# Optimization experiments

Measured on AMD Instinct MI355X. Metric: run time of the kernel, lower is better.

## Reference

```python
import jax, jax.numpy as jnp
import numpy as np

B, S, HID = 2, 4096, 2048
NH, NKV, HD = 16, 4, 128  # num_heads, num_kv_heads, head_dim
GROUPS = NH // NKV
ROPE_THETA = 10000.0


def _rope_cos_sin(position_ids):
    # position_ids: [B, S] int
    inv_freq = 1.0 / (ROPE_THETA ** (jnp.arange(0, HD, 2, dtype=jnp.float32) / HD))  # [HD/2]
    freqs = position_ids.astype(jnp.float32)[..., None] * inv_freq  # [B, S, HD/2]
    emb = jnp.concatenate([freqs, freqs], axis=-1)  # [B, S, HD]
    return jnp.cos(emb), jnp.sin(emb)


def _rotate_half(x):
    x1, x2 = jnp.split(x, 2, axis=-1)
    return jnp.concatenate([-x2, x1], axis=-1)


def _apply_rope(q, k, cos, sin):
    # q: [B, NH, S, HD], k: [B, NKV, S, HD]; cos/sin: [B, S, HD]
    cos = cos[:, None, :, :]
    sin = sin[:, None, :, :]
    q = q * cos + _rotate_half(q) * sin
    k = k * cos + _rotate_half(k) * sin
    return q, k


def kappa(x):
    return jax.nn.elu(x) + 1.0


def setup_inputs() -> dict:
    key = jax.random.key(0)
    ks = jax.random.split(key, 8)
    sc = 0.02
    hidden_states = jax.random.normal(ks[0], (B, S, HID), dtype=jnp.float32)
    position_ids = jnp.broadcast_to(jnp.arange(S, dtype=jnp.int64)[None, :], (B, S))
    Wq = jax.random.normal(ks[1], (HID, NH * HD), dtype=jnp.float32) * sc
    Wk = jax.random.normal(ks[2], (HID, NKV * HD), dtype=jnp.float32) * sc
    Wv = jax.random.normal(ks[3], (HID, NKV * HD), dtype=jnp.float32) * sc
    Wo = jax.random.normal(ks[4], (HID, HID), dtype=jnp.float32) * sc
    Wphi = jax.random.normal(ks[5], (HID, HID), dtype=jnp.float32) * sc
    bphi = jax.random.normal(ks[6], (HID,), dtype=jnp.float32) * sc
    return {"hidden_states": hidden_states, "position_ids": position_ids,
            "Wq": Wq, "Wk": Wk, "Wv": Wv, "Wo": Wo, "Wphi": Wphi, "bphi": bphi}


def reference(hidden_states, position_ids, Wq, Wk, Wv, Wo, Wphi, bphi):
    b, s, _ = hidden_states.shape
    # projections -> [B, heads, S, HD]
    q = (hidden_states @ Wq).reshape(b, s, NH, HD).transpose(0, 2, 1, 3)
    k = (hidden_states @ Wk).reshape(b, s, NKV, HD).transpose(0, 2, 1, 3)
    v = (hidden_states @ Wv).reshape(b, s, NKV, HD).transpose(0, 2, 1, 3)
    cos, sin = _rope_cos_sin(position_ids)
    q, k = _apply_rope(q, k, cos, sin)
    # GQA expand kv heads
    k = jnp.repeat(k, GROUPS, axis=1)  # [B, NH, S, HD]
    v = jnp.repeat(v, GROUPS, axis=1)
    Qk = kappa(q)
    Kk = kappa(k)
    Qg = Qk.mean(axis=2)  # [B, NH, HD]
    logits = jnp.einsum('bnd,bnsd->bns', Qg, Kk)
    alpha = jax.nn.softmax(logits, axis=-1) * float(s)  # [B, NH, S]
    outer_sum = jnp.einsum('bns,bnsd,bnsf->bndf', alpha, Kk, v)  # [B, NH, HD, HD]
    X_phi = (hidden_states @ Wphi + bphi).reshape(b, s, NH, HD).transpose(0, 2, 1, 3)
    result_attn = jnp.einsum('bnsd,bndf->bnsf', Qk, outer_sum)
    context = (X_phi * result_attn).transpose(0, 2, 1, 3).reshape(b, s, HID)
    return context @ Wo
```

## Files before the change

kernel.cpp:

```cpp
#include <hip/hip_runtime.h>
#include <hip/hip_bf16.h>
#include <math.h>

#define B_    2
#define S_    4096
#define HID_  2048
#define NH_   16
#define NKV_  4
#define HD_   128
#define GROUPS_ (NH_/NKV_)
#define ROPE_THETA_ 10000.0f
#define OSPLIT 8
#define QCH   32

typedef __attribute__((ext_vector_type(8))) short short8;
typedef __attribute__((ext_vector_type(4))) float f32x4;

__device__ inline unsigned short f2bf(float f) {
    __hip_bfloat16 h = __float2bfloat16(f);
    return *(unsigned short*)&h;
}

__device__ inline float bf2f(short u) {
    union { unsigned int i; float f; } v;
    v.i = ((unsigned int)(unsigned short)u) << 16;
    return v.f;
}

__device__ inline void gload16(const void* g, void* l) {
    __builtin_amdgcn_global_load_lds((const __attribute__((address_space(1))) void*)g,
                                     (__attribute__((address_space(3))) void*)l, 16, 0, 0);
}

#define BARM() asm volatile("s_barrier" ::: "memory")

__global__ void rope_table_kernel(float* __restrict__ cosT, float* __restrict__ sinT) {
    int s = blockIdx.x;
    int i = threadIdx.x;
    float expo = -2.0f * (float)i / (float)HD_;
    float invf = powf(ROPE_THETA_, expo);
    float f = (float)s * invf;
    cosT[s * 64 + i] = cosf(f);
    sinT[s * 64 + i] = sinf(f);
}

__global__ void cast_bf16_kernel(const float* __restrict__ in,
                                 __hip_bfloat16* __restrict__ out, int n8) {
    int i = blockIdx.x * 256 + threadIdx.x;
    if (i >= n8) return;
    const float4 v0 = *reinterpret_cast<const float4*>(&in[i * 8]);
    const float4 v1 = *reinterpret_cast<const float4*>(&in[i * 8 + 4]);
    union { short8 v; unsigned short u[8]; } o;
    o.u[0] = f2bf(v0.x); o.u[1] = f2bf(v0.y); o.u[2] = f2bf(v0.z); o.u[3] = f2bf(v0.w);
    o.u[4] = f2bf(v1.x); o.u[5] = f2bf(v1.y); o.u[6] = f2bf(v1.z); o.u[7] = f2bf(v1.w);
    *reinterpret_cast<short8*>(&out[i * 8]) = o.v;
}

__global__ __launch_bounds__(256) void transpose_cast_all_kernel(
        const float* __restrict__ Wq, const float* __restrict__ Wphi,
        const float* __restrict__ Wk, const float* __restrict__ Wv,
        const float* __restrict__ Wo, __hip_bfloat16* __restrict__ dstBase) {
    __shared__ float T[64][65];
    int id = blockIdx.x;
    const float* W; int N; size_t dof;
    if (id < 1024)      { W = Wq;   N = 2048; dof = 0; }
    else if (id < 2048) { W = Wphi; N = 2048; dof = (size_t)2048 * HID_;        id -= 1024; }
    else if (id < 2304) { W = Wk;   N = 512;  dof = (size_t)4096 * HID_;        id -= 2048; }
    else if (id < 2560) { W = Wv;   N = 512;  dof = (size_t)(4096 + 512) * HID_; id -= 2304; }
    else                { W = Wo;   N = 2048; dof = (size_t)5120 * HID_;        id -= 2560; }
    __hip_bfloat16* Wt = dstBase + dof;
    int nb = N >> 6;
    int n0 = (id % nb) * 64, k0 = (id / nb) * 64;
    int tid = threadIdx.x;
    int r = tid >> 4, c4 = (tid & 15) * 4;
#pragma unroll
    for (int p = 0; p < 4; ++p) {
        float4 v = *reinterpret_cast<const float4*>(&W[(size_t)(k0 + r + p * 16) * N + n0 + c4]);
        T[r + p * 16][c4 + 0] = v.x;
        T[r + p * 16][c4 + 1] = v.y;
        T[r + p * 16][c4 + 2] = v.z;
        T[r + p * 16][c4 + 3] = v.w;
    }
    __syncthreads();
#pragma unroll
    for (int p = 0; p < 4; ++p) {
        int n = r + p * 16;
        short4 o;
        o.x = (short)f2bf(T[c4 + 0][n]);
        o.y = (short)f2bf(T[c4 + 1][n]);
        o.z = (short)f2bf(T[c4 + 2][n]);
        o.w = (short)f2bf(T[c4 + 3][n]);
        *reinterpret_cast<short4*>(&Wt[(size_t)(n0 + n) * HID_ + k0 + c4]) = o;
    }
}

__device__ __forceinline__ void stage_region128(const __hip_bfloat16* __restrict__ src,
        int ldK, int row0, int kbase, __hip_bfloat16* dst, int tid) {
#pragma unroll
    for (int g = 0; g < 2; ++g) {
        int P = g * 256 + tid;
        int row = P >> 2, cp = P & 3;
        int cl = cp ^ ((row >> 1) & 3);
        gload16(src + (size_t)(row0 + row) * ldK + kbase + cl * 8, dst + P * 8);
    }
}

#define BM 128
#define BN 128
#define T128EL 8192
__global__ __launch_bounds__(256) void gemm_mfma_kernel(
        const __hip_bfloat16* __restrict__ A, const __hip_bfloat16* __restrict__ Bt,
        __hip_bfloat16* __restrict__ Cb, int M, int N, int K) {
    __shared__ __hip_bfloat16 lds[4 * T128EL];
    int tid  = threadIdx.x;
    int wid  = tid >> 6, lane = tid & 63;
    int wr   = wid >> 1, wc = wid & 1;
    int lr = lane & 15, lc = lane >> 4;
    int c16 = lc ^ ((lr >> 1) & 3);
    int bm = blockIdx.y * BM, bn = blockIdx.x * BN;

    f32x4 acc[4][4];
#pragma unroll
    for (int m = 0; m < 4; ++m)
#pragma unroll
        for (int n = 0; n < 4; ++n)
#pragma unroll
            for (int i = 0; i < 4; ++i) acc[m][n][i] = 0.0f;

    const int NKT = K >> 5;

    stage_region128(A,  K, bm, 0,  lds,                 tid);
    stage_region128(Bt, K, bn, 0,  lds + 4096,          tid);
    stage_region128(A,  K, bm, 32, lds + T128EL,        tid);
    stage_region128(Bt, K, bn, 32, lds + T128EL + 4096, tid);
    asm volatile("s_waitcnt vmcnt(4)" ::: "memory");
    BARM();

    for (int kt = 0; kt < NKT; ++kt) {
        __hip_bfloat16* buf = lds + (size_t)(kt & 3) * T128EL;
        __hip_bfloat16* stg = lds + (size_t)((kt + 2) & 3) * T128EL;
        const bool pf = (kt + 2 < NKT);
        if (pf) {
            stage_region128(A,  K, bm, (kt + 2) << 5, stg,        tid);
            stage_region128(Bt, K, bn, (kt + 2) << 5, stg + 4096, tid);
        }
        short8 af[4], bf[4];
#pragma unroll
        for (int m = 0; m < 4; ++m)
            af[m] = *reinterpret_cast<const short8*>(
                &buf[(size_t)(wr * 64 + m * 16 + lr) * 32 + c16 * 8]);
#pragma unroll
        for (int n = 0; n < 4; ++n)
            bf[n] = *reinterpret_cast<const short8*>(
                &buf[4096 + (size_t)(wc * 64 + n * 16 + lr) * 32 + c16 * 8]);
        __builtin_amdgcn_s_setprio(1);
#pragma unroll
        for (int m = 0; m < 4; ++m)
#pragma unroll
            for (int n = 0; n < 4; ++n)
                acc[m][n] = __builtin_amdgcn_mfma_f32_16x16x32_bf16(
                    af[m], bf[n], acc[m][n], 0, 0, 0);
        __builtin_amdgcn_s_setprio(0);
        if (pf) { asm volatile("s_waitcnt vmcnt(4)" ::: "memory"); }
        else    { asm volatile("s_waitcnt vmcnt(0)" ::: "memory"); }
        BARM();
    }

    int lq = lane >> 4;
#pragma unroll
    for (int m = 0; m < 4; ++m) {
#pragma unroll
        for (int n = 0; n < 4; ++n) {
            int row = bm + wr * 64 + m * 16 + lq * 4;
            int col = bn + wc * 64 + n * 16 + lr;
#pragma unroll
            for (int r = 0; r < 4; ++r)
                Cb[(size_t)(row + r) * N + col] = __float2bfloat16(acc[m][n][r]);
        }
    }
}

#define HBUF 32768

__device__ __forceinline__ void stageA64(const __hip_bfloat16* __restrict__ A,
        int ldK, int bm, int k0, __hip_bfloat16* dst, int g, int tid) {
    int P = g * 512 + tid;
    int row = P >> 3, sp = P & 7;
    gload16(A + (size_t)(bm + row) * ldK + k0 + ((sp ^ (row & 7)) << 3),
            dst + (size_t)P * 8);
}
__device__ __forceinline__ void stageB64(const __hip_bfloat16* __restrict__ Bt,
        int ldK, int bn, int k0, __hip_bfloat16* dst, int g, int tid) {
    int P = g * 512 + tid;
    int row = P >> 3, sp = P & 7;
    gload16(Bt + (size_t)(bn + row) * ldK + k0 + ((sp ^ (row & 7)) << 3),
            dst + 16384 + (size_t)P * 8);
}

__device__ __forceinline__ short8 ldsA64(const __hip_bfloat16* buf, int row, int slot_log) {
    int sp = slot_log ^ (row & 7);
    return *reinterpret_cast<const short8*>(&buf[(size_t)row * 64 + sp * 8]);
}
__device__ __forceinline__ short8 ldsB64(const __hip_bfloat16* buf, int row, int slot_log) {
    int sp = slot_log ^ (row & 7);
    return *reinterpret_cast<const short8*>(&buf[16384 + (size_t)row * 64 + sp * 8]);
}

__global__ __launch_bounds__(512, 2) void gemm_mfma256_kernel(
        const __hip_bfloat16* __restrict__ A, const __hip_bfloat16* __restrict__ Bt,
        float* __restrict__ C, __hip_bfloat16* __restrict__ CbQ,
        __hip_bfloat16* __restrict__ CbP, const float* __restrict__ bias,
        int M, int N, int K) {
    __shared__ __hip_bfloat16 lds[2 * HBUF];
    int tid = threadIdx.x, lane = tid & 63, wid = tid >> 6;
    int wr = wid >> 2, wc = wid & 3;
    int lr = lane & 15, lc = lane >> 4;

    int nwg = gridDim.x;
    int orig = blockIdx.x;
    int q = nwg >> 3, r = nwg & 7;
    int xcd = orig & 7, lid = orig >> 3;
    int wg = (xcd < r ? xcd * (q + 1) : r * (q + 1) + (xcd - r) * q) + lid;
    int tiles_n = N >> 8;
    int bm = (wg / tiles_n) << 8, bn = (wg % tiles_n) << 8;

    f32x4 acc[8][4];
#pragma unroll
    for (int m = 0; m < 8; ++m)
#pragma unroll
        for (int n = 0; n < 4; ++n)
#pragma unroll
            for (int i = 0; i < 4; ++i) acc[m][n][i] = 0.0f;

    const int NKT = K >> 6;
    __hip_bfloat16* buf0 = lds;
    __hip_bfloat16* buf1 = lds + HBUF;

#pragma unroll
    for (int g = 0; g < 4; ++g) stageA64(A, K, bm, 0, buf0, g, tid);
#pragma unroll
    for (int g = 0; g < 4; ++g) stageB64(Bt, K, bn, 0, buf0, g, tid);
    stageA64(A, K, bm, 64, buf1, 0, tid);
    stageA64(A, K, bm, 64, buf1, 1, tid);
    asm volatile("s_waitcnt vmcnt(2)" ::: "memory");
    BARM();

    for (int kt = 0; kt < NKT; ++kt) {
        __hip_bfloat16* buf = (kt & 1) ? buf1 : buf0;
        __hip_bfloat16* nxt = (kt & 1) ? buf0 : buf1;
        const bool p1 = (kt + 1 < NKT), p2 = (kt + 2 < NKT);
        const int kn1 = (kt + 1) << 6;

        short8 al[4], ah[4], bl[2], bh[2];

#pragma unroll
        for (int kk = 0; kk < 2; ++kk) {
            int sl = kk * 4 + lc;
#pragma unroll
            for (int m = 0; m < 4; ++m)
                al[m] = ldsA64(buf, wr * 128 + m * 16 + lr, sl);
#pragma unroll
            for (int n = 0; n < 2; ++n)
                bl[n] = ldsB64(buf, wc * 64 + n * 16 + lr, sl);
            if (kk == 0 && p1) {
                stageA64(A, K, bm, kn1, nxt, 2, tid);
                stageA64(A, K, bm, kn1, nxt, 3, tid);
                stageB64(Bt, K, bn, kn1, nxt, 0, tid);
            }
            BARM();
            __builtin_amdgcn_s_setprio(1);
#pragma unroll
            for (int m = 0; m < 4; ++m)
#pragma unroll
                for (int n = 0; n < 2; ++n)
                    acc[m][n] = __builtin_amdgcn_mfma_f32_16x16x32_bf16(
                        al[m], bl[n], acc[m][n], 0, 0, 0);
            __builtin_amdgcn_s_setprio(0);
            BARM();
#pragma unroll
            for (int m = 0; m < 4; ++m)
                ah[m] = ldsA64(buf, wr * 128 + 64 + m * 16 + lr, sl);
            if (kk == 0 && p1) {
                stageB64(Bt, K, bn, kn1, nxt, 1, tid);
                stageB64(Bt, K, bn, kn1, nxt, 2, tid);
                stageB64(Bt, K, bn, kn1, nxt, 3, tid);
            }
            BARM();
            __builtin_amdgcn_s_setprio(1);
#pragma unroll
            for (int m = 0; m < 4; ++m)
#pragma unroll
                for (int n = 0; n < 2; ++n)
                    acc[m + 4][n] = __builtin_amdgcn_mfma_f32_16x16x32_bf16(
                        ah[m], bl[n], acc[m + 4][n], 0, 0, 0);
            __builtin_amdgcn_s_setprio(0);
            BARM();
#pragma unroll
            for (int n = 0; n < 2; ++n)
                bh[n] = ldsB64(buf, wc * 64 + (n + 2) * 16 + lr, sl);
            BARM();
            __builtin_amdgcn_s_setprio(1);
#pragma unroll
            for (int m = 0; m < 4; ++m)
#pragma unroll
                for (int n = 0; n < 2; ++n)
                    acc[m][n + 2] = __builtin_amdgcn_mfma_f32_16x16x32_bf16(
                        al[m], bh[n], acc[m][n + 2], 0, 0, 0);
            __builtin_amdgcn_s_setprio(0);
            BARM();
            if (kk == 1 && p2) {
                stageA64(A, K, bm, (kt + 2) << 6, buf, 0, tid);
                stageA64(A, K, bm, (kt + 2) << 6, buf, 1, tid);
            }
            __builtin_amdgcn_s_setprio(1);
#pragma unroll
            for (int m = 0; m < 4; ++m)
#pragma unroll
                for (int n = 0; n < 2; ++n)
                    acc[m + 4][n + 2] = __builtin_amdgcn_mfma_f32_16x16x32_bf16(
                        ah[m], bh[n], acc[m + 4][n + 2], 0, 0, 0);
            __builtin_amdgcn_s_setprio(0);
            if (kk == 1) {
                if (p2)      { asm volatile("s_waitcnt vmcnt(2)" ::: "memory"); }
                else if (p1) { asm volatile("s_waitcnt vmcnt(0)" ::: "memory"); }
                BARM();
            } else {
                BARM();
            }
        }
    }

    int lq = lane >> 4;
    if (CbQ != nullptr) {
        bool isQ = (bn < 2048);
        __hip_bfloat16* dst = isQ ? CbQ : CbP;
        int cb = isQ ? bn : bn - 2048;
#pragma unroll
        for (int m = 0; m < 8; ++m) {
#pragma unroll
            for (int n = 0; n < 4; ++n) {
                int row = bm + wr * 128 + m * 16 + lq * 4;
                int col = cb + wc * 64 + n * 16 + lr;
                float bv = isQ ? 0.0f : bias[col];
#pragma unroll
                for (int rr = 0; rr < 4; ++rr)
                    dst[(size_t)(row + rr) * 2048 + col] = __float2bfloat16(acc[m][n][rr] + bv);
            }
        }
    } else {
#pragma unroll
        for (int m = 0; m < 8; ++m) {
#pragma unroll
            for (int n = 0; n < 4; ++n) {
                int row = bm + wr * 128 + m * 16 + lq * 4;
                int col = bn + wc * 64 + n * 16 + lr;
#pragma unroll
                for (int rr = 0; rr < 4; ++rr)
                    C[(size_t)(row + rr) * N + col] = acc[m][n][rr];
            }
        }
    }
}

__global__ __launch_bounds__(256) void rope_qg_kernel(
        __hip_bfloat16* __restrict__ Qb, const float* __restrict__ cosT,
        const float* __restrict__ sinT, float* __restrict__ QPART) {
    int blk = blockIdx.x;
    int c = blk % QCH, bn = blk / QCH;
    int b = bn / NH_, n = bn % NH_;
    int tid = threadIdx.x;
    int pg = tid & 7;
    int sg = tid >> 3;
    int s0 = c * (S_ / QCH);
    float acc1[8] = {}, acc2[8] = {};
    for (int sr = sg; sr < S_ / QCH; sr += 32) {
        int s = s0 + sr;
        size_t base = ((size_t)b * S_ + s) * (NH_ * HD_) + n * HD_ + pg * 8;
        short8 v1 = *reinterpret_cast<short8*>(&Qb[base]);
        short8 v2 = *reinterpret_cast<short8*>(&Qb[base + 64]);
        union { short8 v; unsigned short u[8]; } o1, o2;
#pragma unroll
        for (int j = 0; j < 8; ++j) {
            float cc = cosT[s * 64 + pg * 8 + j];
            float ss = sinT[s * 64 + pg * 8 + j];
            float x1 = bf2f(v1[j]), x2 = bf2f(v2[j]);
            float r1 = x1 * cc - x2 * ss;
            float r2 = x2 * cc + x1 * ss;
            r1 = (r1 > 0.0f) ? (r1 + 1.0f) : expf(r1);
            r2 = (r2 > 0.0f) ? (r2 + 1.0f) : expf(r2);
            o1.u[j] = f2bf(r1);
            o2.u[j] = f2bf(r2);
            acc1[j] += bf2f((short)o1.u[j]);
            acc2[j] += bf2f((short)o2.u[j]);
        }
        *reinterpret_cast<short8*>(&Qb[base])      = o1.v;
        *reinterpret_cast<short8*>(&Qb[base + 64]) = o2.v;
    }
    __shared__ float red[32][128];
#pragma unroll
    for (int j = 0; j < 8; ++j) {
        red[sg][pg * 8 + j]      = acc1[j];
        red[sg][64 + pg * 8 + j] = acc2[j];
    }
    __syncthreads();
    if (tid < 128) {
        float s = 0.0f;
#pragma unroll
        for (int g = 0; g < 32; ++g) s += red[g][tid];
        QPART[(size_t)(c * (B_ * NH_) + bn) * HD_ + tid] = s;
    }
}

__global__ __launch_bounds__(256) void qg_reduce_kernel(
        const float* __restrict__ QPART, float* __restrict__ QG) {
    int idx = blockIdx.x * 256 + threadIdx.x;
    float acc = 0.0f;
#pragma unroll
    for (int c = 0; c < QCH; ++c)
        acc += QPART[(size_t)c * (B_ * NH_ * HD_) + idx];
    QG[idx] = acc * (1.0f / (float)S_);
}

__global__ void rope_kappa_b_kernel(__hip_bfloat16* __restrict__ Xb,
                                    const float* __restrict__ cosT,
                                    const float* __restrict__ sinT,
                                    int nheads, int rs, int total) {
    int idx = blockIdx.x * 256 + threadIdx.x;
    if (idx >= total) return;
    int dq = idx & 15;
    int t  = idx >> 4;
    int n  = t % nheads;
    int bs = t / nheads;
    int s  = bs % S_;
    size_t base = (size_t)bs * rs + n * HD_ + dq * 4;
    short4 v1 = *reinterpret_cast<short4*>(&Xb[base]);
    short4 v2 = *reinterpret_cast<short4*>(&Xb[base + 64]);
    float4 c4 = *reinterpret_cast<const float4*>(&cosT[s * 64 + dq * 4]);
    float4 s4 = *reinterpret_cast<const float4*>(&sinT[s * 64 + dq * 4]);
    float x1[4] = {bf2f(v1.x), bf2f(v1.y), bf2f(v1.z), bf2f(v1.w)};
    float x2[4] = {bf2f(v2.x), bf2f(v2.y), bf2f(v2.z), bf2f(v2.w)};
    float cc[4] = {c4.x, c4.y, c4.z, c4.w};
    float ss[4] = {s4.x, s4.y, s4.z, s4.w};
    short r1s[4], r2s[4];
#pragma unroll
    for (int j = 0; j < 4; ++j) {
        float r1 = x1[j] * cc[j] - x2[j] * ss[j];
        float r2 = x2[j] * cc[j] + x1[j] * ss[j];
        r1 = (r1 > 0.0f) ? (r1 + 1.0f) : expf(r1);
        r2 = (r2 > 0.0f) ? (r2 + 1.0f) : expf(r2);
        r1s[j] = (short)f2bf(r1);
        r2s[j] = (short)f2bf(r2);
    }
    short4 o1, o2;
    o1.x = r1s[0]; o1.y = r1s[1]; o1.z = r1s[2]; o1.w = r1s[3];
    o2.x = r2s[0]; o2.y = r2s[1]; o2.z = r2s[2]; o2.w = r2s[3];
    *reinterpret_cast<short4*>(&Xb[base])      = o1;
    *reinterpret_cast<short4*>(&Xb[base + 64]) = o2;
}

__global__ __launch_bounds__(256) void logits_kernel(
        const __hip_bfloat16* __restrict__ KVb, const float* __restrict__ QG,
        float* __restrict__ LG) {
    int bk = blockIdx.x;
    int b = bk / NKV_, kn = bk % NKV_;
    int s0 = blockIdx.y * 256;
    int w = threadIdx.x >> 6, lane = threadIdx.x & 63;
    float2 qv[GROUPS_];
#pragma unroll
    for (int g = 0; g < GROUPS_; ++g)
        qv[g] = *reinterpret_cast<const float2*>(
            &QG[(size_t)(b * NH_ + kn * GROUPS_ + g) * HD_ + lane * 2]);
    for (int i = 0; i < 64; ++i) {
        int s = s0 + w * 64 + i;
        short2 kv = *reinterpret_cast<const short2*>(
            &KVb[((size_t)b * S_ + s) * 1024 + kn * HD_ + lane * 2]);
        float kx = bf2f(kv.x), ky = bf2f(kv.y);
        float p[GROUPS_];
#pragma unroll
        for (int g = 0; g < GROUPS_; ++g) p[g] = kx * qv[g].x + ky * qv[g].y;
#pragma unroll
        for (int off = 32; off > 0; off >>= 1)
#pragma unroll
            for (int g = 0; g < GROUPS_; ++g) p[g] += __shfl_xor(p[g], off);
        if (lane == 0) {
#pragma unroll
            for (int g = 0; g < GROUPS_; ++g)
                LG[(size_t)(b * NH_ + kn * GROUPS_ + g) * S_ + s] = p[g];
        }
    }
}

__global__ __launch_bounds__(1024) void softmax_alpha_kernel(float* __restrict__ LG) {
    int bn = blockIdx.x;
    float* row = &LG[(size_t)bn * S_];
    __shared__ float lg[S_];
    __shared__ float red[1024];
    int tid = threadIdx.x;
    float lmax = -1e30f;
    for (int s = tid; s < S_; s += 1024) {
        float v = row[s];
        lg[s] = v;
        lmax = fmaxf(lmax, v);
    }
    red[tid] = lmax;
    __syncthreads();
    for (int off = 512; off > 0; off >>= 1) {
        if (tid < off) red[tid] = fmaxf(red[tid], red[tid + off]);
        __syncthreads();
    }
    float mx = red[0];
    __syncthreads();
    float lsum = 0.0f;
    for (int s = tid; s < S_; s += 1024) {
        float e = expf(lg[s] - mx);
        lg[s] = e;
        lsum += e;
    }
    red[tid] = lsum;
    __syncthreads();
    for (int off = 512; off > 0; off >>= 1) {
        if (tid < off) red[tid] += red[tid + off];
        __syncthreads();
    }
    float inv = (float)S_ / red[0];
    for (int s = tid; s < S_; s += 1024)
        row[s] = lg[s] * inv;
}

__global__ __launch_bounds__(256) void kvt_kernel(
        const __hip_bfloat16* __restrict__ KVb, const float* __restrict__ ALPHA,
        __hip_bfloat16* __restrict__ AKT, __hip_bfloat16* __restrict__ VT) {
    int bk = blockIdx.x;
    int b = bk / NKV_, kn = bk % NKV_;
    int s0 = blockIdx.y * 64;
    int isV = blockIdx.z;
    __shared__ float T[64][HD_ + 4];
    __shared__ float alf[GROUPS_][64];
    int tid = threadIdx.x;

    int r = tid >> 2;
    int c0 = (tid & 3) * 32;
    const __hip_bfloat16* src =
        KVb + ((size_t)(b * S_) + s0 + r) * 1024 + isV * 512 + kn * HD_ + c0;
#pragma unroll
    for (int i = 0; i < 4; ++i) {
        short8 v = *reinterpret_cast<const short8*>(src + i * 8);
#pragma unroll
        for (int j = 0; j < 8; ++j) T[r][c0 + i * 8 + j] = bf2f(v[j]);
    }
    if (!isV) {
        int g = tid >> 6, ss = tid & 63;
        alf[g][ss] = ALPHA[(size_t)(b * NH_ + kn * GROUPS_ + g) * S_ + s0 + ss];
    }
    __syncthreads();

    int d  = tid >> 1;
    int sh = (tid & 1) * 32;
    if (isV) {
        __hip_bfloat16* dst = VT + ((size_t)bk * HD_ + d) * S_ + s0 + sh;
#pragma unroll
        for (int i = 0; i < 8; ++i) {
            short4 o;
            o.x = (short)f2bf(T[sh + i * 4 + 0][d]);
            o.y = (short)f2bf(T[sh + i * 4 + 1][d]);
            o.z = (short)f2bf(T[sh + i * 4 + 2][d]);
            o.w = (short)f2bf(T[sh + i * 4 + 3][d]);
            *reinterpret_cast<short4*>(dst + i * 4) = o;
        }
    } else {
#pragma unroll
        for (int g = 0; g < GROUPS_; ++g) {
            int n = kn * GROUPS_ + g;
            __hip_bfloat16* dst = AKT + ((size_t)(b * NH_ + n) * HD_ + d) * S_ + s0 + sh;
#pragma unroll
            for (int i = 0; i < 8; ++i) {
                short4 o;
                o.x = (short)f2bf(T[sh + i * 4 + 0][d] * alf[g][sh + i * 4 + 0]);
                o.y = (short)f2bf(T[sh + i * 4 + 1][d] * alf[g][sh + i * 4 + 1]);
                o.z = (short)f2bf(T[sh + i * 4 + 2][d] * alf[g][sh + i * 4 + 2]);
                o.w = (short)f2bf(T[sh + i * 4 + 3][d] * alf[g][sh + i * 4 + 3]);
                *reinterpret_cast<short4*>(dst + i * 4) = o;
            }
        }
    }
}

__global__ __launch_bounds__(256) void outer_mfma_kernel(
        const __hip_bfloat16* __restrict__ AKT, const __hip_bfloat16* __restrict__ VT,
        float* __restrict__ OPT) {
    int bn = blockIdx.x;
    int sp = blockIdx.y;
    int b = bn / NH_, n = bn % NH_;
    int kn = n / GROUPS_;
    const __hip_bfloat16* Abase = AKT + (size_t)bn * HD_ * S_ + sp * (S_ / OSPLIT);
    const __hip_bfloat16* Bbase = VT + (size_t)(b * NKV_ + kn) * HD_ * S_ + sp * (S_ / OSPLIT);
    __shared__ __hip_bfloat16 As[128 * 32];
    __shared__ __hip_bfloat16 Bs[128 * 32];
    int tid = threadIdx.x, lane = tid & 63, wid = tid >> 6;
    int wr = wid >> 1, wc = wid & 1;
    int lr = lane & 15, kq = (lane >> 4) * 8;

    f32x4 acc[4][4];
#pragma unroll
    for (int m = 0; m < 4; ++m)
#pragma unroll
        for (int nn = 0; nn < 4; ++nn)
#pragma unroll
            for (int i = 0; i < 4; ++i) acc[m][nn][i] = 0.0f;

    for (int ks = 0; ks < (S_ / OSPLIT) / 32; ++ks) {
        int k0 = ks * 32;
#pragma unroll
        for (int g = 0; g < 2; ++g) {
            int P = g * 256 + tid;
            int row = P >> 2, gr = P & 3;
            gload16(Abase + (size_t)row * S_ + k0 + gr * 8, As + P * 8);
            gload16(Bbase + (size_t)row * S_ + k0 + gr * 8, Bs + P * 8);
        }
        __syncthreads();
        short8 af[4], bf[4];
#pragma unroll
        for (int m = 0; m < 4; ++m)
            af[m] = *reinterpret_cast<short8*>(&As[(wr * 64 + m * 16 + lr) * 32 + kq]);
#pragma unroll
        for (int nn = 0; nn < 4; ++nn)
            bf[nn] = *reinterpret_cast<short8*>(&Bs[(wc * 64 + nn * 16 + lr) * 32 + kq]);
#pragma unroll
        for (int m = 0; m < 4; ++m)
#pragma unroll
            for (int nn = 0; nn < 4; ++nn)
                acc[m][nn] = __builtin_amdgcn_mfma_f32_16x16x32_bf16(
                    af[m], bf[nn], acc[m][nn], 0, 0, 0);
        __syncthreads();
    }

    float* base = OPT + ((size_t)bn * OSPLIT + sp) * (HD_ * HD_);
    int lq = lane >> 4;
#pragma unroll
    for (int m = 0; m < 4; ++m) {
#pragma unroll
        for (int nn = 0; nn < 4; ++nn) {
            int drow = wr * 64 + m * 16 + lq * 4;
            int fcol = wc * 64 + nn * 16 + lr;
            float4 o;
            o.x = acc[m][nn][0]; o.y = acc[m][nn][1];
            o.z = acc[m][nn][2]; o.w = acc[m][nn][3];
            *reinterpret_cast<float4*>(&base[(size_t)fcol * HD_ + drow]) = o;
        }
    }
}

__global__ __launch_bounds__(256) void outer_reduce_tc_kernel(
        const float* __restrict__ OPT, __hip_bfloat16* __restrict__ OUTt) {
    int idx = blockIdx.x * 256 + threadIdx.x;
    int bn = idx >> 11;
    int rem = idx & 2047;
    int f = rem >> 4, g = rem & 15;
    const float* src = OPT + (size_t)bn * OSPLIT * 16384 + f * 128 + g * 8;
    float s[8] = {};
#pragma unroll
    for (int sp = 0; sp < OSPLIT; ++sp) {
        float4 v0 = *reinterpret_cast<const float4*>(src + (size_t)sp * 16384);
        float4 v1 = *reinterpret_cast<const float4*>(src + (size_t)sp * 16384 + 4);
        s[0] += v0.x; s[1] += v0.y; s[2] += v0.z; s[3] += v0.w;
        s[4] += v1.x; s[5] += v1.y; s[6] += v1.z; s[7] += v1.w;
    }
    int gp = g ^ (f & 7);
    union { short8 v; unsigned short u[8]; } o;
#pragma unroll
    for (int j = 0; j < 8; ++j) o.u[j] = f2bf(s[j]);
    *reinterpret_cast<short8*>(&OUTt[(size_t)bn * 16384 + f * 128 + gp * 8]) = o.v;
}

__global__ __launch_bounds__(256) void attn_context_mfma_kernel(
        const __hip_bfloat16* __restrict__ Qb, const __hip_bfloat16* __restrict__ OUTt,
        const __hip_bfloat16* __restrict__ XPHIb, __hip_bfloat16* __restrict__ CTX) {
    int bn = blockIdx.x;
    int b = bn / NH_, n = bn % NH_;
    int s0 = blockIdx.y * 256;
    __shared__ __hip_bfloat16 Ms[128 * 128];
    int tid = threadIdx.x, lane = tid & 63, wid = tid >> 6;
    int lr = lane & 15, lc = lane >> 4;

#pragma unroll
    for (int g = 0; g < 8; ++g) {
        int P = g * 256 + tid;
        gload16(OUTt + (size_t)bn * 16384 + (size_t)P * 8, Ms + (size_t)P * 8);
    }

    f32x4 acc[4][8];
#pragma unroll
    for (int m = 0; m < 4; ++m)
#pragma unroll
        for (int nn = 0; nn < 8; ++nn)
#pragma unroll
            for (int i = 0; i < 4; ++i) acc[m][nn][i] = 0.0f;

    __syncthreads();

    const __hip_bfloat16* qbase =
        Qb + ((size_t)(b * S_) + s0 + wid * 64) * (NH_ * HD_) + n * HD_;
#pragma unroll
    for (int ks = 0; ks < 4; ++ks) {
        int k8 = ks * 32 + lc * 8;
        short8 a[4];
#pragma unroll
        for (int m = 0; m < 4; ++m)
            a[m] = *reinterpret_cast<const short8*>(
                qbase + (size_t)(m * 16 + lr) * (NH_ * HD_) + k8);
        int gfull = ks * 4 + lc;
        short8 bb[8];
#pragma unroll
        for (int nn = 0; nn < 8; ++nn) {
            int f = nn * 16 + lr;
            int gp = gfull ^ (f & 7);
            bb[nn] = *reinterpret_cast<const short8*>(&Ms[f * 128 + gp * 8]);
        }
#pragma unroll
        for (int m = 0; m < 4; ++m)
#pragma unroll
            for (int nn = 0; nn < 8; ++nn)
                acc[m][nn] = __builtin_amdgcn_mfma_f32_16x16x32_bf16(
                    a[m], bb[nn], acc[m][nn], 0, 0, 0);
    }

#pragma unroll
    for (int m = 0; m < 4; ++m) {
#pragma unroll
        for (int nn = 0; nn < 8; ++nn) {
            int row = s0 + wid * 64 + m * 16 + lc * 4;
            int f = nn * 16 + lr;
            size_t gi = ((size_t)(b * S_) + row) * (NH_ * HD_) + n * HD_ + f;
#pragma unroll
            for (int r = 0; r < 4; ++r) {
                float xp = __bfloat162float(XPHIb[gi + (size_t)r * (NH_ * HD_)]);
                CTX[gi + (size_t)r * (NH_ * HD_)] = __float2bfloat16(acc[m][nn][r] * xp);
            }
        }
    }
}

extern "C" void kernel_launch(void* const* d_in, const int* in_sizes, int n_in,
                              void* d_out, int out_size, void* d_ws, size_t ws_size,
                              hipStream_t stream) {
    (void)in_sizes; (void)n_in; (void)out_size; (void)ws_size;
    const float* X    = (const float*)d_in[0];
    const float* Wq   = (const float*)d_in[2];
    const float* Wk   = (const float*)d_in[3];
    const float* Wv   = (const float*)d_in[4];
    const float* Wo   = (const float*)d_in[5];
    const float* Wphi = (const float*)d_in[6];
    const float* bphi = (const float*)d_in[7];
    float* out = (float*)d_out;

    float* ws = (float*)d_ws;
    const size_t nQ = (size_t)B_ * S_ * NH_ * HD_;
    const size_t nK = (size_t)B_ * S_ * NKV_ * HD_;
    float* Q     = ws;
    float* KV    = Q + nQ;
    float* XPHI  = KV + 2 * nK;
    float* QG    = XPHI + nQ;
    float* ALPHA = QG + (size_t)B_ * NH_ * HD_;
    float* QPART = ALPHA + (size_t)B_ * NH_ * S_;
    float* COST  = QPART + (size_t)QCH * B_ * NH_ * HD_;
    float* SINT  = COST + (size_t)S_ * 64;
    __hip_bfloat16* Xb     = (__hip_bfloat16*)(SINT + (size_t)S_ * 64);
    __hip_bfloat16* WqPhit = Xb + nQ;
    __hip_bfloat16* Wkt    = WqPhit + (size_t)4096 * HID_;
    __hip_bfloat16* Wot    = WqPhit + (size_t)5120 * HID_;
    __hip_bfloat16* OUTt   = Wot + (size_t)HID_ * HID_;
    __hip_bfloat16* VT     = OUTt + (size_t)B_ * NH_ * HD_ * HD_;
    float* OPT = (float*)(VT + nK);
    __hip_bfloat16* Qb    = (__hip_bfloat16*)Q;
    __hip_bfloat16* KVb   = (__hip_bfloat16*)KV;
    __hip_bfloat16* CTXb  = (__hip_bfloat16*)KV;
    __hip_bfloat16* AKT   = Xb;
    __hip_bfloat16* XPHIb = (__hip_bfloat16*)XPHI;

    const int M = B_ * S_;

    rope_table_kernel<<<S_, 64, 0, stream>>>(COST, SINT);
    cast_bf16_kernel<<<(int)(nQ / 8 / 256), 256, 0, stream>>>(X, Xb, (int)(nQ / 8));
    transpose_cast_all_kernel<<<3584, 256, 0, stream>>>(Wq, Wphi, Wk, Wv, Wo, WqPhit);

    gemm_mfma256_kernel<<<(M / 256) * (4096 / 256), 512, 0, stream>>>(
        Xb, WqPhit, nullptr, Qb, XPHIb, bphi, M, 4096, HID_);
    gemm_mfma_kernel<<<dim3(1024 / BN, M / BM), 256, 0, stream>>>(
        Xb, Wkt, KVb, M, 1024, HID_);

    rope_qg_kernel<<<B_ * NH_ * QCH, 256, 0, stream>>>(Qb, COST, SINT, QPART);
    {
        int totalK = B_ * S_ * NKV_ * 16;
        rope_kappa_b_kernel<<<totalK / 256, 256, 0, stream>>>(
            KVb, COST, SINT, NKV_, 1024, totalK);
    }

    qg_reduce_kernel<<<(B_ * NH_ * HD_) / 256, 256, 0, stream>>>(QPART, QG);
    logits_kernel<<<dim3(B_ * NKV_, S_ / 256), 256, 0, stream>>>(KVb, QG, ALPHA);
    softmax_alpha_kernel<<<B_ * NH_, 1024, 0, stream>>>(ALPHA);

    kvt_kernel<<<dim3(B_ * NKV_, S_ / 64, 2), 256, 0, stream>>>(KVb, ALPHA, AKT, VT);
    outer_mfma_kernel<<<dim3(B_ * NH_, OSPLIT), 256, 0, stream>>>(AKT, VT, OPT);
    outer_reduce_tc_kernel<<<(B_ * NH_ * HD_ * 16) / 256, 256, 0, stream>>>(OPT, OUTt);

    attn_context_mfma_kernel<<<dim3(B_ * NH_, S_ / 256), 256, 0, stream>>>(
        Qb, OUTt, XPHIb, CTXb);

    gemm_mfma256_kernel<<<(M / 256) * (HID_ / 256), 512, 0, stream>>>(
        CTXb, Wot, out, nullptr, nullptr, nullptr, M, HID_, HID_);
}
```

Before: 409.7 us.

## Restructure GEMM main loop into four phases with both k-halves per phase

Reorganizes the 256x256 MFMA GEMM inner loop so each phase loads both 32-wide k-slices of A and B fragments and issues paired MFMAs, cutting the number of LDS-read/barrier phases per k-tile from eight to four. Global prefetch staging is regrouped into A and B halves, with the next-next tile's B half now prefetched earlier into the current buffer, and the vmcnt waits are adjusted. An explicit lgkmcnt(0) wait and sched_barrier are added after each barrier. This is meant to reduce barrier and synchronization overhead and to overlap global loads better with compute. In exchange it raises register pressure from holding more fragments, which matters under the 512-thread, 2-blocks launch bound.

```diff
diff --git a/kernel.cpp b/kernel.cpp
--- a/kernel.cpp
+++ b/kernel.cpp
@@ -206,6 +206,19 @@
     return *reinterpret_cast<const short8*>(&buf[16384 + (size_t)row * 64 + sp * 8]);
 }
 
+#define STAGE_A1(kt, dst) { stageA64(A, K, bm, (kt) << 6, dst, 0, tid); \
+                            stageA64(A, K, bm, (kt) << 6, dst, 1, tid); }
+#define STAGE_A2(kt, dst) { stageA64(A, K, bm, (kt) << 6, dst, 2, tid); \
+                            stageA64(A, K, bm, (kt) << 6, dst, 3, tid); }
+#define STAGE_B1(kt, dst) { stageB64(Bt, K, bn, (kt) << 6, dst, 0, tid); \
+                            stageB64(Bt, K, bn, (kt) << 6, dst, 1, tid); }
+#define STAGE_B2(kt, dst) { stageB64(Bt, K, bn, (kt) << 6, dst, 2, tid); \
+                            stageB64(Bt, K, bn, (kt) << 6, dst, 3, tid); }
+
+#define PHASE_SYNC() do { BARM(); \
+    asm volatile("s_waitcnt lgkmcnt(0)" ::: "memory"); \
+    __builtin_amdgcn_sched_barrier(0); } while (0)
+
 __global__ __launch_bounds__(512, 2) void gemm_mfma256_kernel(
         const __hip_bfloat16* __restrict__ A, const __hip_bfloat16* __restrict__ Bt,
         float* __restrict__ C, __hip_bfloat16* __restrict__ CbQ,
@@ -236,98 +249,94 @@
     __hip_bfloat16* buf0 = lds;
     __hip_bfloat16* buf1 = lds + HBUF;
 
-#pragma unroll
-    for (int g = 0; g < 4; ++g) stageA64(A, K, bm, 0, buf0, g, tid);
-#pragma unroll
-    for (int g = 0; g < 4; ++g) stageB64(Bt, K, bn, 0, buf0, g, tid);
-    stageA64(A, K, bm, 64, buf1, 0, tid);
-    stageA64(A, K, bm, 64, buf1, 1, tid);
-    asm volatile("s_waitcnt vmcnt(2)" ::: "memory");
+    STAGE_B1(0, buf0); STAGE_A1(0, buf0); STAGE_A2(0, buf0); STAGE_B2(0, buf0);
+    STAGE_B1(1, buf1); STAGE_A1(1, buf1);
+    asm volatile("s_waitcnt vmcnt(4)" ::: "memory");
     BARM();
 
     for (int kt = 0; kt < NKT; ++kt) {
         __hip_bfloat16* buf = (kt & 1) ? buf1 : buf0;
         __hip_bfloat16* nxt = (kt & 1) ? buf0 : buf1;
         const bool p1 = (kt + 1 < NKT), p2 = (kt + 2 < NKT);
-        const int kn1 = (kt + 1) << 6;
-
-        short8 al[4], ah[4], bl[2], bh[2];
-
-#pragma unroll
-        for (int kk = 0; kk < 2; ++kk) {
-            int sl = kk * 4 + lc;
-#pragma unroll
-            for (int m = 0; m < 4; ++m)
-                al[m] = ldsA64(buf, wr * 128 + m * 16 + lr, sl);
+
+        short8 a[4][2], blo[2][2], bhi[2][2];
+
+#pragma unroll
+        for (int m = 0; m < 4; ++m)
+#pragma unroll
+            for (int kk = 0; kk < 2; ++kk)
+                a[m][kk] = ldsA64(buf, wr * 128 + m * 16 + lr, kk * 4 + lc);
+#pragma unroll
+        for (int n = 0; n < 2; ++n)
+#pragma unroll
+            for (int kk = 0; kk < 2; ++kk)
+                blo[n][kk] = ldsB64(buf, wc * 64 + n * 16 + lr, kk * 4 + lc);
+        if (p1) STAGE_A2(kt + 1, nxt);
+        PHASE_SYNC();
+        __builtin_amdgcn_s_setprio(1);
+#pragma unroll
+        for (int m = 0; m < 4; ++m)
 #pragma unroll
             for (int n = 0; n < 2; ++n)
-                bl[n] = ldsB64(buf, wc * 64 + n * 16 + lr, sl);
-            if (kk == 0 && p1) {
-                stageA64(A, K, bm, kn1, nxt, 2, tid);
-                stageA64(A, K, bm, kn1, nxt, 3, tid);
-                stageB64(Bt, K, bn, kn1, nxt, 0, tid);
-            }
-            BARM();
-            __builtin_amdgcn_s_setprio(1);
-#pragma unroll
-            for (int m = 0; m < 4; ++m)
-#pragma unroll
-                for (int n = 0; n < 2; ++n)
+#pragma unroll
+                for (int kk = 0; kk < 2; ++kk)
                     acc[m][n] = __builtin_amdgcn_mfma_f32_16x16x32_bf16(
-                        al[m], bl[n], acc[m][n], 0, 0, 0);
-            __builtin_amdgcn_s_setprio(0);
-            BARM();
-#pragma unroll
-            for (int m = 0; m < 4; ++m)
-                ah[m] = ldsA64(buf, wr * 128 + 64 + m * 16 + lr, sl);
-            if (kk == 0 && p1) {
-                stageB64(Bt, K, bn, kn1, nxt, 1, tid);
-                stageB64(Bt, K, bn, kn1, nxt, 2, tid);
-                stageB64(Bt, K, bn, kn1, nxt, 3, tid);
-            }
-            BARM();
-            __builtin_amdgcn_s_setprio(1);
-#pragma unroll
-            for (int m = 0; m < 4; ++m)
-#pragma unroll
-                for (int n = 0; n < 2; ++n)
+                        a[m][kk], blo[n][kk], acc[m][n], 0, 0, 0);
+        __builtin_amdgcn_s_setprio(0);
+        BARM();
+
+#pragma unroll
+        for (int n = 0; n < 2; ++n)
+#pragma unroll
+            for (int kk = 0; kk < 2; ++kk)
+                bhi[n][kk] = ldsB64(buf, wc * 64 + (n + 2) * 16 + lr, kk * 4 + lc);
+        if (p1) STAGE_B2(kt + 1, nxt);
+        PHASE_SYNC();
+        __builtin_amdgcn_s_setprio(1);
+#pragma unroll
+        for (int m = 0; m < 4; ++m)
+#pragma unroll
+            for (int n = 0; n < 2; ++n)
+#pragma unroll
+                for (int kk = 0; kk < 2; ++kk)
+                    acc[m][n + 2] = __builtin_amdgcn_mfma_f32_16x16x32_bf16(
+                        a[m][kk], bhi[n][kk], acc[m][n + 2], 0, 0, 0);
+        __builtin_amdgcn_s_setprio(0);
+        BARM();
+
+#pragma unroll
+        for (int m = 0; m < 4; ++m)
+#pragma unroll
+            for (int kk = 0; kk < 2; ++kk)
+                a[m][kk] = ldsA64(buf, wr * 128 + 64 + m * 16 + lr, kk * 4 + lc);
+        if (p2) STAGE_B1(kt + 2, buf);
+        PHASE_SYNC();
+        __builtin_amdgcn_s_setprio(1);
+#pragma unroll
+        for (int m = 0; m < 4; ++m)
+#pragma unroll
+            for (int n = 0; n < 2; ++n)
+#pragma unroll
+                for (int kk = 0; kk < 2; ++kk)
                     acc[m + 4][n] = __builtin_amdgcn_mfma_f32_16x16x32_bf16(
-                        ah[m], bl[n], acc[m + 4][n], 0, 0, 0);
-            __builtin_amdgcn_s_setprio(0);
-            BARM();
+                        a[m][kk], blo[n][kk], acc[m + 4][n], 0, 0, 0);
+        __builtin_amdgcn_s_setprio(0);
+        BARM();
+
+        if (p2) STAGE_A1(kt + 2, buf);
+        __builtin_amdgcn_s_setprio(1);
+#pragma unroll
+        for (int m = 0; m < 4; ++m)
 #pragma unroll
             for (int n = 0; n < 2; ++n)
-                bh[n] = ldsB64(buf, wc * 64 + (n + 2) * 16 + lr, sl);
-            BARM();
-            __builtin_amdgcn_s_setprio(1);
-#pragma unroll
-            for (int m = 0; m < 4; ++m)
-#pragma unroll
-                for (int n = 0; n < 2; ++n)
-                    acc[m][n + 2] = __builtin_amdgcn_mfma_f32_16x16x32_bf16(
-                        al[m], bh[n], acc[m][n + 2], 0, 0, 0);
-            __builtin_amdgcn_s_setprio(0);
-            BARM();
-            if (kk == 1 && p2) {
-                stageA64(A, K, bm, (kt + 2) << 6, buf, 0, tid);
-                stageA64(A, K, bm, (kt + 2) << 6, buf, 1, tid);
-            }
-            __builtin_amdgcn_s_setprio(1);
-#pragma unroll
-            for (int m = 0; m < 4; ++m)
-#pragma unroll
-                for (int n = 0; n < 2; ++n)
+#pragma unroll
+                for (int kk = 0; kk < 2; ++kk)
                     acc[m + 4][n + 2] = __builtin_amdgcn_mfma_f32_16x16x32_bf16(
-                        ah[m], bh[n], acc[m + 4][n + 2], 0, 0, 0);
-            __builtin_amdgcn_s_setprio(0);
-            if (kk == 1) {
-                if (p2)      { asm volatile("s_waitcnt vmcnt(2)" ::: "memory"); }
-                else if (p1) { asm volatile("s_waitcnt vmcnt(0)" ::: "memory"); }
-                BARM();
-            } else {
-                BARM();
-            }
-        }
+                        a[m][kk], bhi[n][kk], acc[m + 4][n + 2], 0, 0, 0);
+        __builtin_amdgcn_s_setprio(0);
+        if (p2)      { asm volatile("s_waitcnt vmcnt(4)" ::: "memory"); }
+        else if (p1) { asm volatile("s_waitcnt vmcnt(0)" ::: "memory"); }
+        BARM();
     }
 
     int lq = lane >> 4;
```

New measurement: 409.0 us (median of 2 runs). About the same (-0.2%).

## Replace 256x256 GEMM kernel with generalized 128x128 MFMA GEMM for all projections

Applied to the files above, without the earlier changes.

Removes the 256x256-tile, 512-thread GEMM with XCD-aware block remapping and uses the 128x128-tile, 256-thread GEMM for the Q/Phi projection and the output projection. The smaller kernel gains an epilogue that can split columns into Q and bias-added Phi outputs, or write fp32. This gives more blocks and a simpler pipeline, but lowers per-block data reuse and drops the XCD-aware L2 locality mapping, which risks higher memory traffic on the large GEMMs.

```diff
diff --git a/kernel.cpp b/kernel.cpp
--- a/kernel.cpp
+++ b/kernel.cpp
@@ -110,7 +110,9 @@
 #define T128EL 8192
 __global__ __launch_bounds__(256) void gemm_mfma_kernel(
         const __hip_bfloat16* __restrict__ A, const __hip_bfloat16* __restrict__ Bt,
-        __hip_bfloat16* __restrict__ Cb, int M, int N, int K) {
+        float* __restrict__ C, __hip_bfloat16* __restrict__ Cq,
+        __hip_bfloat16* __restrict__ Cp, const float* __restrict__ bias,
+        int M, int N, int K) {
     __shared__ __hip_bfloat16 lds[4 * T128EL];
     int tid  = threadIdx.x;
     int wid  = tid >> 6, lane = tid & 63;
@@ -173,190 +175,24 @@
         for (int n = 0; n < 4; ++n) {
             int row = bm + wr * 64 + m * 16 + lq * 4;
             int col = bn + wc * 64 + n * 16 + lr;
-#pragma unroll
-            for (int r = 0; r < 4; ++r)
-                Cb[(size_t)(row + r) * N + col] = __float2bfloat16(acc[m][n][r]);
-        }
-    }
-}
-
-#define HBUF 32768
-
-__device__ __forceinline__ void stageA64(const __hip_bfloat16* __restrict__ A,
-        int ldK, int bm, int k0, __hip_bfloat16* dst, int g, int tid) {
-    int P = g * 512 + tid;
-    int row = P >> 3, sp = P & 7;
-    gload16(A + (size_t)(bm + row) * ldK + k0 + ((sp ^ (row & 7)) << 3),
-            dst + (size_t)P * 8);
-}
-__device__ __forceinline__ void stageB64(const __hip_bfloat16* __restrict__ Bt,
-        int ldK, int bn, int k0, __hip_bfloat16* dst, int g, int tid) {
-    int P = g * 512 + tid;
-    int row = P >> 3, sp = P & 7;
-    gload16(Bt + (size_t)(bn + row) * ldK + k0 + ((sp ^ (row & 7)) << 3),
-            dst + 16384 + (size_t)P * 8);
-}
-
-__device__ __forceinline__ short8 ldsA64(const __hip_bfloat16* buf, int row, int slot_log) {
-    int sp = slot_log ^ (row & 7);
-    return *reinterpret_cast<const short8*>(&buf[(size_t)row * 64 + sp * 8]);
-}
-__device__ __forceinline__ short8 ldsB64(const __hip_bfloat16* buf, int row, int slot_log) {
-    int sp = slot_log ^ (row & 7);
-    return *reinterpret_cast<const short8*>(&buf[16384 + (size_t)row * 64 + sp * 8]);
-}
-
-__global__ __launch_bounds__(512, 2) void gemm_mfma256_kernel(
-        const __hip_bfloat16* __restrict__ A, const __hip_bfloat16* __restrict__ Bt,
-        float* __restrict__ C, __hip_bfloat16* __restrict__ CbQ,
-        __hip_bfloat16* __restrict__ CbP, const float* __restrict__ bias,
-        int M, int N, int K) {
-    __shared__ __hip_bfloat16 lds[2 * HBUF];
-    int tid = threadIdx.x, lane = tid & 63, wid = tid >> 6;
-    int wr = wid >> 2, wc = wid & 3;
-    int lr = lane & 15, lc = lane >> 4;
-
-    int nwg = gridDim.x;
-    int orig = blockIdx.x;
-    int q = nwg >> 3, r = nwg & 7;
-    int xcd = orig & 7, lid = orig >> 3;
-    int wg = (xcd < r ? xcd * (q + 1) : r * (q + 1) + (xcd - r) * q) + lid;
-    int tiles_n = N >> 8;
-    int bm = (wg / tiles_n) << 8, bn = (wg % tiles_n) << 8;
-
-    f32x4 acc[8][4];
-#pragma unroll
-    for (int m = 0; m < 8; ++m)
-#pragma unroll
-        for (int n = 0; n < 4; ++n)
-#pragma unroll
-            for (int i = 0; i < 4; ++i) acc[m][n][i] = 0.0f;
-
-    const int NKT = K >> 6;
-    __hip_bfloat16* buf0 = lds;
-    __hip_bfloat16* buf1 = lds + HBUF;
-
-#pragma unroll
-    for (int g = 0; g < 4; ++g) stageA64(A, K, bm, 0, buf0, g, tid);
-#pragma unroll
-    for (int g = 0; g < 4; ++g) stageB64(Bt, K, bn, 0, buf0, g, tid);
-    stageA64(A, K, bm, 64, buf1, 0, tid);
-    stageA64(A, K, bm, 64, buf1, 1, tid);
-    asm volatile("s_waitcnt vmcnt(2)" ::: "memory");
-    BARM();
-
-    for (int kt = 0; kt < NKT; ++kt) {
-        __hip_bfloat16* buf = (kt & 1) ? buf1 : buf0;
-        __hip_bfloat16* nxt = (kt & 1) ? buf0 : buf1;
-        const bool p1 = (kt + 1 < NKT), p2 = (kt + 2 < NKT);
-        const int kn1 = (kt + 1) << 6;
-
-        short8 al[4], ah[4], bl[2], bh[2];
-
-#pragma unroll
-        for (int kk = 0; kk < 2; ++kk) {
-            int sl = kk * 4 + lc;
-#pragma unroll
-            for (int m = 0; m < 4; ++m)
-                al[m] = ldsA64(buf, wr * 128 + m * 16 + lr, sl);
-#pragma unroll
-            for (int n = 0; n < 2; ++n)
-                bl[n] = ldsB64(buf, wc * 64 + n * 16 + lr, sl);
-            if (kk == 0 && p1) {
-                stageA64(A, K, bm, kn1, nxt, 2, tid);
-                stageA64(A, K, bm, kn1, nxt, 3, tid);
-                stageB64(Bt, K, bn, kn1, nxt, 0, tid);
-            }
-            BARM();
-            __builtin_amdgcn_s_setprio(1);
-#pragma unroll
-            for (int m = 0; m < 4; ++m)
-#pragma unroll
-                for (int n = 0; n < 2; ++n)
-                    acc[m][n] = __builtin_amdgcn_mfma_f32_16x16x32_bf16(
-                        al[m], bl[n], acc[m][n], 0, 0, 0);
-            __builtin_amdgcn_s_setprio(0);
-            BARM();
-#pragma unroll
-            for (int m = 0; m < 4; ++m)
-                ah[m] = ldsA64(buf, wr * 128 + 64 + m * 16 + lr, sl);
-            if (kk == 0 && p1) {
-                stageB64(Bt, K, bn, kn1, nxt, 1, tid);
-                stageB64(Bt, K, bn, kn1, nxt, 2, tid);
-                stageB64(Bt, K, bn, kn1, nxt, 3, tid);
-            }
-            BARM();
-            __builtin_amdgcn_s_setprio(1);
-#pragma unroll
-            for (int m = 0; m < 4; ++m)
-#pragma unroll
-                for (int n = 0; n < 2; ++n)
-                    acc[m + 4][n] = __builtin_amdgcn_mfma_f32_16x16x32_bf16(
-                        ah[m], bl[n], acc[m + 4][n], 0, 0, 0);
-            __builtin_amdgcn_s_setprio(0);
-            BARM();
-#pragma unroll
-            for (int n = 0; n < 2; ++n)
-                bh[n] = ldsB64(buf, wc * 64 + (n + 2) * 16 + lr, sl);
-            BARM();
-            __builtin_amdgcn_s_setprio(1);
-#pragma unroll
-            for (int m = 0; m < 4; ++m)
-#pragma unroll
-                for (int n = 0; n < 2; ++n)
-                    acc[m][n + 2] = __builtin_amdgcn_mfma_f32_16x16x32_bf16(
-                        al[m], bh[n], acc[m][n + 2], 0, 0, 0);
-            __builtin_amdgcn_s_setprio(0);
-            BARM();
-            if (kk == 1 && p2) {
-                stageA64(A, K, bm, (kt + 2) << 6, buf, 0, tid);
-                stageA64(A, K, bm, (kt + 2) << 6, buf, 1, tid);
-            }
-            __builtin_amdgcn_s_setprio(1);
-#pragma unroll
-            for (int m = 0; m < 4; ++m)
-#pragma unroll
-                for (int n = 0; n < 2; ++n)
-                    acc[m + 4][n + 2] = __builtin_amdgcn_mfma_f32_16x16x32_bf16(
-                        ah[m], bh[n], acc[m + 4][n + 2], 0, 0, 0);
-            __builtin_amdgcn_s_setprio(0);
-            if (kk == 1) {
-                if (p2)      { asm volatile("s_waitcnt vmcnt(2)" ::: "memory"); }
-                else if (p1) { asm volatile("s_waitcnt vmcnt(0)" ::: "memory"); }
-                BARM();
+            if (Cq != nullptr) {
+                __hip_bfloat16* dst; int cc, ldc; float bv = 0.0f;
+                if (Cp != nullptr) {
+                    bool isQ = (col < 2048);
+                    dst = isQ ? Cq : Cp;
+                    cc = isQ ? col : col - 2048;
+                    ldc = 2048;
+                    if (!isQ) bv = bias[cc];
+                } else {
+                    dst = Cq; cc = col; ldc = N;
+                }
+#pragma unroll
+                for (int r = 0; r < 4; ++r)
+                    dst[(size_t)(row + r) * ldc + cc] = __float2bfloat16(acc[m][n][r] + bv);
             } else {
-                BARM();
-            }
-        }
-    }
-
-    int lq = lane >> 4;
-    if (CbQ != nullptr) {
-        bool isQ = (bn < 2048);
-        __hip_bfloat16* dst = isQ ? CbQ : CbP;
-        int cb = isQ ? bn : bn - 2048;
-#pragma unroll
-        for (int m = 0; m < 8; ++m) {
-#pragma unroll
-            for (int n = 0; n < 4; ++n) {
-                int row = bm + wr * 128 + m * 16 + lq * 4;
-                int col = cb + wc * 64 + n * 16 + lr;
-                float bv = isQ ? 0.0f : bias[col];
-#pragma unroll
-                for (int rr = 0; rr < 4; ++rr)
-                    dst[(size_t)(row + rr) * 2048 + col] = __float2bfloat16(acc[m][n][rr] + bv);
-            }
-        }
-    } else {
-#pragma unroll
-        for (int m = 0; m < 8; ++m) {
-#pragma unroll
-            for (int n = 0; n < 4; ++n) {
-                int row = bm + wr * 128 + m * 16 + lq * 4;
-                int col = bn + wc * 64 + n * 16 + lr;
-#pragma unroll
-                for (int rr = 0; rr < 4; ++rr)
-                    C[(size_t)(row + rr) * N + col] = acc[m][n][rr];
+#pragma unroll
+                for (int r = 0; r < 4; ++r)
+                    C[(size_t)(row + r) * N + col] = acc[m][n][r];
             }
         }
     }
@@ -783,10 +619,10 @@
     cast_bf16_kernel<<<(int)(nQ / 8 / 256), 256, 0, stream>>>(X, Xb, (int)(nQ / 8));
     transpose_cast_all_kernel<<<3584, 256, 0, stream>>>(Wq, Wphi, Wk, Wv, Wo, WqPhit);
 
-    gemm_mfma256_kernel<<<(M / 256) * (4096 / 256), 512, 0, stream>>>(
+    gemm_mfma_kernel<<<dim3(4096 / BN, M / BM), 256, 0, stream>>>(
         Xb, WqPhit, nullptr, Qb, XPHIb, bphi, M, 4096, HID_);
     gemm_mfma_kernel<<<dim3(1024 / BN, M / BM), 256, 0, stream>>>(
-        Xb, Wkt, KVb, M, 1024, HID_);
+        Xb, Wkt, nullptr, KVb, nullptr, nullptr, M, 1024, HID_);
 
     rope_qg_kernel<<<B_ * NH_ * QCH, 256, 0, stream>>>(Qb, COST, SINT, QPART);
     {
@@ -806,6 +642,6 @@
     attn_context_mfma_kernel<<<dim3(B_ * NH_, S_ / 256), 256, 0, stream>>>(
         Qb, OUTt, XPHIb, CTXb);
 
-    gemm_mfma256_kernel<<<(M / 256) * (HID_ / 256), 512, 0, stream>>>(
+    gemm_mfma_kernel<<<dim3(HID_ / BN, M / BM), 256, 0, stream>>>(
         CTXb, Wot, out, nullptr, nullptr, nullptr, M, HID_, HID_);
 }
```

Measured after the change: 458.5 us. 1.12x slower.
